# Kernel optimization log

Hardware: AMD Instinct MI355X
Metric: run time of the kernel (lower is better)

The kernel has to match this reference:

```python
import jax, jax.numpy as jnp
import numpy as np

L = 2        # n_layers
F = 128      # in_features == out_features (GRUCell + highway constraint)
O = 128
N = 1024     # nodes
B = 8        # batch
D = 3        # edge directions (weight.size(0))


def setup_inputs() -> dict:
    key = jax.random.key(0)
    ks = jax.random.split(key, 10)
    s = 1.0 / np.sqrt(F)
    u = lambda k, shp: jax.random.uniform(k, shp, jnp.float32, minval=-s, maxval=s)
    return {
        "inputs": jax.random.normal(ks[0], (N, B, F), jnp.float32),
        "adj": jax.random.uniform(ks[1], (D, B, N, N), jnp.float32),
        "W": u(ks[2], (L, D, F, O)),            # GCN weight per layer/direction
        "Bc": u(ks[3], (L, D, O)),              # GCN bias
        "Wh": u(ks[4], (L, F, O)),              # highway weight
        "Bh": u(ks[5], (L, O)),                 # highway bias
        "Wih": u(ks[6], (L, 3 * O, O)),         # GRUCell input weights
        "Whh": u(ks[7], (L, 3 * O, O)),         # GRUCell hidden weights
        "bih": u(ks[8], (L, 3 * O)),
        "bhh": u(ks[9], (L, 3 * O)),
    }


def _gru(x, h, wih, whh, bih, bhh):
    # torch.nn.GRUCell semantics; x,h: [..., O]
    gi = x @ wih.T + bih
    gh = h @ whh.T + bhh
    i_r, i_z, i_n = jnp.split(gi, 3, axis=-1)
    h_r, h_z, h_n = jnp.split(gh, 3, axis=-1)
    r = jax.nn.sigmoid(i_r + h_r)
    z = jax.nn.sigmoid(i_z + h_z)
    n = jnp.tanh(i_n + r * h_n)
    return (1.0 - z) * n + z * h


def reference(inputs, adj, W, Bc, Wh, Bh, Wih, Whh, bih, bhh):
    x = inputs  # [N, B, F]; dropout layers are identity at eval
    for l in range(L):
        # support per direction: [D, B, N, O]
        support = jnp.einsum('nbf,dfo->dbno', x, W[l]) + Bc[l][:, None, None, :]
        # adjacency-weighted aggregation: adj[d,b] @ support[d,b]
        agg = jnp.einsum('dbmn,dbno->dbmo', adj, support)
        # GRU update with hidden = current features, per direction, summed over d
        h = jnp.broadcast_to(jnp.transpose(x, (1, 0, 2))[None], agg.shape)
        hnew = _gru(agg, h, Wih[l], Whh[l], bih[l], bhh[l])
        out = jnp.transpose(jnp.sum(hnew, axis=0), (1, 0, 2))  # [N, B, O]
        out = jax.nn.relu(out)  # activation='relu'
        # highway gate (highway='relu')
        t = jax.nn.relu(jnp.einsum('nbf,fo->nbo', x, Wh[l]) + Bh[l])
        x = out * t + x * (1.0 - t)
    return x
```

## Files before the change

kernel.cpp:

```cpp
#include <hip/hip_runtime.h>
#include <math.h>

#define N_NODES 1024
#define BATCH   8
#define FEAT    128
#define NDIR    3
#define NB      (N_NODES*BATCH)
#define G3      384

typedef __bf16 bf16_t;
using bf16x8 = __attribute__((ext_vector_type(8))) __bf16;
using bf16x4 = __attribute__((ext_vector_type(4))) __bf16;
using f32x4  = __attribute__((ext_vector_type(4))) float;

#define GLOAD_LDS16(g, l) \
    __builtin_amdgcn_global_load_lds((const __attribute__((address_space(1))) void*)(g), \
                                     (__attribute__((address_space(3))) void*)(l), 16, 0, 0)

template<int R>
__device__ __forceinline__ void stage_swz(const bf16_t* __restrict__ src, int stride,
                                          int k0, bf16_t* lds, int w, int lane)
{
    #pragma unroll
    for (int q = 0; q < R/32; ++q) {
        int rbase = w*(R/4) + q*8;
        int row = rbase + (lane >> 3);
        int seg = (lane & 7) ^ (row & 7);
        GLOAD_LDS16(src + (size_t)row*stride + k0 + seg*8,
                    (char*)lds + (size_t)rbase*128);
    }
}

__device__ __forceinline__ void stageA_f32(const float* __restrict__ src, int k0,
                                           bf16_t* lds, bf16_t* __restrict__ gout,
                                           int w, int lane)
{
    #pragma unroll
    for (int q = 0; q < 2; ++q) {
        int rbase = w*16 + q*8;
        int row = rbase + (lane >> 3);
        int s   = lane & 7;
        int seg = s ^ (row & 7);
        const float* g = src + (size_t)row*1024 + k0 + seg*8;
        float4 v0 = *reinterpret_cast<const float4*>(g);
        float4 v1 = *reinterpret_cast<const float4*>(g + 4);
        bf16x8 pk;
        pk[0]=(bf16_t)(v0.x-0.5f); pk[1]=(bf16_t)(v0.y-0.5f);
        pk[2]=(bf16_t)(v0.z-0.5f); pk[3]=(bf16_t)(v0.w-0.5f);
        pk[4]=(bf16_t)(v1.x-0.5f); pk[5]=(bf16_t)(v1.y-0.5f);
        pk[6]=(bf16_t)(v1.z-0.5f); pk[7]=(bf16_t)(v1.w-0.5f);
        *reinterpret_cast<bf16x8*>(&lds[row*64 + s*8]) = pk;
        *reinterpret_cast<bf16x8*>(gout + (size_t)row*1024 + k0 + seg*8) = pk;
    }
}

template<int MI, int NJ>
__device__ __forceinline__ void mfma_swz(const bf16_t* As, const bf16_t* Bs,
                                         f32x4 (&acc)[MI][NJ], int wr, int wc, int lane)
{
    #pragma unroll
    for (int ks = 0; ks < 64; ks += 32) {
        int bslot = ks/8 + (lane >> 4);
        int sx = bslot ^ (lane & 7);
        bf16x8 af[MI], bfv[NJ];
        #pragma unroll
        for (int i = 0; i < MI; ++i) {
            int row = wr*MI*16 + i*16 + (lane & 15);
            af[i] = *reinterpret_cast<const bf16x8*>(&As[row*64 + sx*8]);
        }
        #pragma unroll
        for (int j = 0; j < NJ; ++j) {
            int row = wc*NJ*16 + j*16 + (lane & 15);
            bfv[j] = *reinterpret_cast<const bf16x8*>(&Bs[row*64 + sx*8]);
        }
        #pragma unroll
        for (int i = 0; i < MI; ++i) {
            #pragma unroll
            for (int j = 0; j < NJ; ++j)
                acc[i][j] = __builtin_amdgcn_mfma_f32_16x16x32_bf16(af[i], bfv[j], acc[i][j], 0, 0, 0);
        }
    }
}

__global__ __launch_bounds__(128) void k_wprep(
    const float* __restrict__ W, const float* __restrict__ Wh,
    const float* __restrict__ Whh, const float* __restrict__ Wih,
    bf16_t* __restrict__ wsup,
    bf16_t* __restrict__ wihc)
{
    int m = blockIdx.x, l = blockIdx.y, k = threadIdx.x;
    float w;
    bf16_t* dst;
    bool patB = false;
    if (m < 384) {
        int d = m >> 7, o = m & 127;
        w = W[((size_t)(l*3 + d)*128 + k)*128 + o];
        dst = wsup + ((size_t)l*896 + m)*384;
    } else if (m < 512) {
        int o = m - 384;
        w = Wh[((size_t)l*128 + k)*128 + o];
        dst = wsup + ((size_t)l*896 + m)*384;
    } else if (m < 896) {
        int c = m - 512;
        w = Whh[((size_t)l*384 + c)*128 + k];
        dst = wsup + ((size_t)l*896 + m)*384;
    } else {
        int c = m - 896;
        w = Wih[((size_t)l*384 + c)*128 + k];
        dst = wihc + ((size_t)l*384 + c)*384;
        patB = true;
    }
    bf16_t hi = (bf16_t)w;
    bf16_t lo = (bf16_t)(w - (float)hi);
    if (patB) { dst[k] = hi; dst[128 + k] = hi; dst[256 + k] = lo; }
    else      { dst[k] = hi; dst[128 + k] = lo; dst[256 + k] = hi; }
}

__global__ __launch_bounds__(256) void k_xcat(
    const float* __restrict__ X, bf16_t* __restrict__ xcat)
{
    int idx = blockIdx.x * 256 + threadIdx.x;
    int k = idx & 127, r = idx >> 7;
    int n = r >> 3, b = r & 7;
    float v = X[idx];
    bf16_t hi = (bf16_t)v;
    bf16_t lo = (bf16_t)(v - (float)hi);
    bf16_t* dst = xcat + ((size_t)(b*1024 + n))*384 + k;
    dst[0] = hi; dst[128] = hi; dst[256] = lo;
}

__global__ __launch_bounds__(256, 2) void k_sup2(
    const bf16_t* __restrict__ Wcat,
    const bf16_t* __restrict__ xcat,
    const float* __restrict__ Bcl,
    const float* __restrict__ Bhl,
    const float* __restrict__ bhhl,
    bf16_t* __restrict__ supt,
    float* __restrict__ tbuf,
    bf16_t* __restrict__ ghb)
{
    __shared__ bf16_t As[2][128*64];
    __shared__ bf16_t Bs[2][128*64];
    const int t = threadIdx.x, lane = t & 63, w = t >> 6;
    const int wr = w >> 1, wc = w & 1;
    const int n0 = blockIdx.x * 128;
    const int m0 = blockIdx.y * 128;
    const int b  = blockIdx.z;
    const bf16_t* Arow = Wcat + (size_t)m0 * 384;
    const bf16_t* Brow = xcat + ((size_t)b * 1024 + n0) * 384;

    f32x4 acc[4][4] = {};
    stage_swz<128>(Arow, 384, 0, As[0], w, lane);
    stage_swz<128>(Brow, 384, 0, Bs[0], w, lane);
    __syncthreads();
    #pragma unroll
    for (int kt = 0; kt < 6; ++kt) {
        if (kt + 1 < 6) {
            stage_swz<128>(Arow, 384, (kt+1)*64, As[(kt+1)&1], w, lane);
            stage_swz<128>(Brow, 384, (kt+1)*64, Bs[(kt+1)&1], w, lane);
        }
        mfma_swz<4,4>(As[kt&1], Bs[kt&1], acc, wr, wc, lane);
        __syncthreads();
    }
    #pragma unroll
    for (int i = 0; i < 4; ++i) {
        int mb = m0 + wr*64 + i*16 + ((lane >> 4) * 4);
        #pragma unroll
        for (int j = 0; j < 4; ++j) {
            int n = n0 + wc*64 + j*16 + (lane & 15);
            if (mb < 384) {
                #pragma unroll
                for (int rg = 0; rg < 4; ++rg) {
                    int m = mb + rg;
                    int d = m >> 7, o = m & 127;
                    supt[((size_t)((d*8 + b)*128 + o))*1024 + n] =
                        (bf16_t)(acc[i][j][rg] + Bcl[d*128 + o]);
                }
            } else if (mb < 512) {
                #pragma unroll
                for (int rg = 0; rg < 4; ++rg) {
                    int o = mb + rg - 384;
                    tbuf[((size_t)(b*128 + o))*1024 + n] =
                        fmaxf(acc[i][j][rg] + Bhl[o], 0.0f);
                }
            } else {
                int c = mb - 512;
                bf16x4 pk;
                #pragma unroll
                for (int rg = 0; rg < 4; ++rg)
                    pk[rg] = (bf16_t)(acc[i][j][rg] + bhhl[c + rg]);
                *reinterpret_cast<bf16x4*>(&ghb[((size_t)(b*1024 + n))*384 + c]) = pk;
            }
        }
    }
}

__global__ __launch_bounds__(256) void k_colsum(
    const bf16_t* __restrict__ supt, float* __restrict__ colsum)
{
    int row = blockIdx.x * 4 + (threadIdx.x >> 6);
    int lane = threadIdx.x & 63;
    const bf16_t* p = supt + (size_t)row * 1024 + lane * 16;
    bf16x8 v0 = *reinterpret_cast<const bf16x8*>(p);
    bf16x8 v1 = *reinterpret_cast<const bf16x8*>(p + 8);
    float s = 0.0f;
    #pragma unroll
    for (int i = 0; i < 8; ++i) s += (float)v0[i] + (float)v1[i];
    #pragma unroll
    for (int off = 32; off > 0; off >>= 1) s += __shfl_down(s, off, 64);
    if (lane == 0) colsum[row] = s;
}

template<int AMODE>
__global__ __launch_bounds__(256, 2) void k_agg(
    const float* __restrict__ adjf,
    bf16_t* __restrict__ adjb,
    const bf16_t* __restrict__ supt,
    const float* __restrict__ colsum,
    bf16_t* __restrict__ aggcat)
{
    __shared__ bf16_t As[2][64*64];
    __shared__ bf16_t Bs[2][128*64];
    const int t = threadIdx.x, lane = t & 63, w = t >> 6;
    const int wr = w >> 1, wc = w & 1;
    const int m0 = blockIdx.x * 64;
    const int z  = blockIdx.y;
    const float*  Af = adjf + (size_t)z * 1024 * 1024 + (size_t)m0 * 1024;
    bf16_t*       Ab = adjb + (size_t)z * 1024 * 1024 + (size_t)m0 * 1024;
    const bf16_t* Brow = supt + (size_t)z * 128 * 1024;

    f32x4 acc[2][4] = {};
    if (AMODE) stageA_f32(Af, 0, As[0], Ab, w, lane);
    else       stage_swz<64>(Ab, 1024, 0, As[0], w, lane);
    stage_swz<128>(Brow, 1024, 0, Bs[0], w, lane);
    __syncthreads();
    #pragma unroll
    for (int kt = 0; kt < 16; ++kt) {
        if (kt + 1 < 16) {
            if (AMODE) stageA_f32(Af, (kt+1)*64, As[(kt+1)&1], Ab, w, lane);
            else       stage_swz<64>(Ab, 1024, (kt+1)*64, As[(kt+1)&1], w, lane);
            stage_swz<128>(Brow, 1024, (kt+1)*64, Bs[(kt+1)&1], w, lane);
        }
        mfma_swz<2,4>(As[kt&1], Bs[kt&1], acc, wr, wc, lane);
        __syncthreads();
    }
    #pragma unroll
    for (int i = 0; i < 2; ++i) {
        #pragma unroll
        for (int rg = 0; rg < 4; ++rg) {
            size_t m = (size_t)z*1024 + m0 + wr*32 + i*16 + ((lane >> 4) * 4) + rg;
            bf16_t* row = aggcat + m*384;
            #pragma unroll
            for (int j = 0; j < 4; ++j) {
                int o = wc*64 + j*16 + (lane & 15);
                float v = acc[i][j][rg] + 0.5f * colsum[z*128 + o];
                bf16_t hi = (bf16_t)v;
                bf16_t lo = (bf16_t)(v - (float)hi);
                row[o] = hi; row[128 + o] = lo; row[256 + o] = hi;
            }
        }
    }
}

__global__ __launch_bounds__(256, 2) void k_gi(
    const bf16_t* __restrict__ A,
    const bf16_t* __restrict__ B,
    const float*  __restrict__ bias,
    bf16_t* __restrict__ girz,
    float* __restrict__ gin)
{
    __shared__ bf16_t As[2][128*64];
    __shared__ bf16_t Bs[2][128*64];
    const int t = threadIdx.x, lane = t & 63, w = t >> 6;
    const int wr = w >> 1, wc = w & 1;
    const int m0 = blockIdx.x * 128;
    const int c0 = blockIdx.y * 128;
    const bf16_t* Arow = A + (size_t)m0 * 384;
    const bf16_t* Brow = B + (size_t)c0 * 384;

    f32x4 acc[4][4] = {};
    stage_swz<128>(Arow, 384, 0, As[0], w, lane);
    stage_swz<128>(Brow, 384, 0, Bs[0], w, lane);
    __syncthreads();
    #pragma unroll
    for (int kt = 0; kt < 6; ++kt) {
        if (kt + 1 < 6) {
            stage_swz<128>(Arow, 384, (kt+1)*64, As[(kt+1)&1], w, lane);
            stage_swz<128>(Brow, 384, (kt+1)*64, Bs[(kt+1)&1], w, lane);
        }
        mfma_swz<4,4>(As[kt&1], Bs[kt&1], acc, wr, wc, lane);
        __syncthreads();
    }
    #pragma unroll
    for (int j = 0; j < 4; ++j) {
        int c = c0 + wc*64 + j*16 + (lane & 15);
        float bv = bias[c];
        #pragma unroll
        for (int i = 0; i < 4; ++i) {
            #pragma unroll
            for (int rg = 0; rg < 4; ++rg) {
                int m = m0 + wr*64 + i*16 + ((lane >> 4) * 4) + rg;
                float v = acc[i][j][rg] + bv;
                if (c < 256) girz[(size_t)m*256 + c] = (bf16_t)v;
                else         gin[(size_t)m*128 + (c - 256)] = v;
            }
        }
    }
}

__global__ __launch_bounds__(256) void k_gates(
    const bf16_t* __restrict__ girz, const float* __restrict__ gin,
    const bf16_t* __restrict__ ghb,
    bf16_t* xcat,
    const float* __restrict__ tbuf,
    float* __restrict__ Xout, int write_xcat)
{
    __shared__ float ts[128*17];
    const int b = blockIdx.y, n0 = blockIdx.x * 16;
    const int tid = threadIdx.x;
    {
        int o = tid >> 1, nh = (tid & 1) * 8;
        const float* src = tbuf + ((size_t)(b*128 + o))*1024 + n0 + nh;
        float4 v0 = *reinterpret_cast<const float4*>(src);
        float4 v1 = *reinterpret_cast<const float4*>(src + 4);
        float* dst = &ts[o*17 + nh];
        dst[0]=v0.x; dst[1]=v0.y; dst[2]=v0.z; dst[3]=v0.w;
        dst[4]=v1.x; dst[5]=v1.y; dst[6]=v1.z; dst[7]=v1.w;
    }
    __syncthreads();
    #pragma unroll
    for (int p = 0; p < 8; ++p) {
        int e = p*256 + tid;
        int nn = e >> 7, o = e & 127;
        int n = n0 + nn;
        size_t rb = (size_t)(b*1024 + n);
        bf16_t* xr = xcat + rb*384;
        float h = (float)xr[o] + (float)xr[256 + o];
        const bf16_t* ghr = ghb + rb*G3;
        float g_r = (float)ghr[o], g_z = (float)ghr[128+o], g_n = (float)ghr[256+o];
        float acc = 0.0f;
        #pragma unroll
        for (int d = 0; d < 3; ++d) {
            size_t rr = (size_t)((d*8 + b)*1024 + n);
            float i_r = (float)girz[rr*256 + o];
            float i_z = (float)girz[rr*256 + 128 + o];
            float i_n = gin[rr*128 + o];
            float rg = 1.0f / (1.0f + expf(-(i_r + g_r)));
            float zg = 1.0f / (1.0f + expf(-(i_z + g_z)));
            float ng = tanhf(i_n + rg * g_n);
            acc += (1.0f - zg) * ng + zg * h;
        }
        float outv = fmaxf(acc, 0.0f);
        float tg = ts[o*17 + nn];
        float res = outv * tg + h * (1.0f - tg);
        if (Xout) Xout[(size_t)(n*8 + b)*128 + o] = res;
        if (write_xcat) {
            bf16_t hi = (bf16_t)res;
            bf16_t lo = (bf16_t)(res - (float)hi);
            xr[o] = hi; xr[128 + o] = hi; xr[256 + o] = lo;
        }
    }
}

extern "C" void kernel_launch(void* const* d_in, const int* in_sizes, int n_in,
                              void* d_out, int out_size, void* d_ws, size_t ws_size,
                              hipStream_t stream) {
    const float* inputs = (const float*)d_in[0];
    const float* adj    = (const float*)d_in[1];
    const float* W      = (const float*)d_in[2];
    const float* Bc     = (const float*)d_in[3];
    const float* Wh     = (const float*)d_in[4];
    const float* Bh     = (const float*)d_in[5];
    const float* Wih    = (const float*)d_in[6];
    const float* Whh    = (const float*)d_in[7];
    const float* bih    = (const float*)d_in[8];
    const float* bhh    = (const float*)d_in[9];

    char* ws = (char*)d_ws;
    float*  tbuf   = (float*)ws;   ws += (size_t)8*128*1024*4;
    bf16_t* xcat   = (bf16_t*)ws;  ws += (size_t)8*1024*384*2;
    bf16_t* ghb    = (bf16_t*)ws;  ws += (size_t)NB*G3*2;
    bf16_t* supt   = (bf16_t*)ws;  ws += (size_t)24*128*1024*2;
    bf16_t* aggcat = (bf16_t*)ws;  ws += (size_t)3*NB*384*2;
    bf16_t* girz   = (bf16_t*)ws;  ws += (size_t)3*NB*256*2;
    float*  gin    = (float*)ws;   ws += (size_t)3*NB*128*4;
    float*  colsum = (float*)ws;   ws += (size_t)24*128*4;
    bf16_t* wsup   = (bf16_t*)ws;  ws += (size_t)2*896*384*2;
    bf16_t* wihc   = (bf16_t*)ws;  ws += (size_t)2*384*384*2;
    bf16_t* adjb   = (bf16_t*)ws;

    k_wprep<<<dim3(1280, 2), dim3(128), 0, stream>>>(W, Wh, Whh, Wih, wsup, wihc);
    k_xcat<<<dim3(4096), dim3(256), 0, stream>>>(inputs, xcat);

    for (int l = 0; l < 2; ++l) {
        k_sup2<<<dim3(8, 7, 8), dim3(256), 0, stream>>>(
            wsup + (size_t)l*896*384, xcat, Bc + l*3*128, Bh + l*128, bhh + l*G3,
            supt, tbuf, ghb);
        k_colsum<<<dim3(768), dim3(256), 0, stream>>>(supt, colsum);
        if (l == 0)
            k_agg<1><<<dim3(16, 24), dim3(256), 0, stream>>>(adj, adjb, supt, colsum, aggcat);
        else
            k_agg<0><<<dim3(16, 24), dim3(256), 0, stream>>>(adj, adjb, supt, colsum, aggcat);
        k_gi<<<dim3(192, 3), dim3(256), 0, stream>>>(
            aggcat, wihc + (size_t)l*384*384, bih + l*G3, girz, gin);
        k_gates<<<dim3(64, 8), dim3(256), 0, stream>>>(
            girz, gin, ghb, xcat, tbuf,
            (l == 1) ? (float*)d_out : (float*)nullptr, (l == 0) ? 1 : 0);
    }
}
```

Measured before the change: 331.9 us.

## Fuse colsum into support GEMM, drop bf16 adj cache, use fast gate math

The column-sum kernel is removed and its reduction is folded into the support GEMM epilogue through wave shuffles and atomicAdd into a buffer zeroed by the xcat kernel. The aggregation kernel now always converts fp32 adjacency on the fly instead of writing a bf16 copy in layer 0 and reading it back in layer 1. Its occupancy hint is raised to 3 blocks per SM, and the GRU gates use exp2/rcp intrinsics in place of expf/tanhf. This saves a kernel launch and the adjb write, but layer 1 now reads fp32 adjacency (twice the bytes), and the atomics make the sums order-dependent.

```diff
diff --git a/kernel.cpp b/kernel.cpp
--- a/kernel.cpp
+++ b/kernel.cpp
@@ -32,8 +32,7 @@
 }
 
 __device__ __forceinline__ void stageA_f32(const float* __restrict__ src, int k0,
-                                           bf16_t* lds, bf16_t* __restrict__ gout,
-                                           int w, int lane)
+                                           bf16_t* lds, int w, int lane)
 {
     #pragma unroll
     for (int q = 0; q < 2; ++q) {
@@ -50,7 +49,6 @@
         pk[4]=(bf16_t)(v1.x-0.5f); pk[5]=(bf16_t)(v1.y-0.5f);
         pk[6]=(bf16_t)(v1.z-0.5f); pk[7]=(bf16_t)(v1.w-0.5f);
         *reinterpret_cast<bf16x8*>(&lds[row*64 + s*8]) = pk;
-        *reinterpret_cast<bf16x8*>(gout + (size_t)row*1024 + k0 + seg*8) = pk;
     }
 }
 
@@ -80,6 +78,19 @@
                 acc[i][j] = __builtin_amdgcn_mfma_f32_16x16x32_bf16(af[i], bfv[j], acc[i][j], 0, 0, 0);
         }
     }
+}
+
+__device__ __forceinline__ float fast_sigmoid(float x)
+{
+    float t = __builtin_amdgcn_exp2f(-1.442695041f * x);
+    return __builtin_amdgcn_rcpf(1.0f + t);
+}
+__device__ __forceinline__ float fast_tanh(float x)
+{
+    float ax = fabsf(x);
+    float t = __builtin_amdgcn_exp2f(-2.885390082f * ax);
+    float r = (1.0f - t) * __builtin_amdgcn_rcpf(1.0f + t);
+    return copysignf(r, x);
 }
 
 __global__ __launch_bounds__(128) void k_wprep(
@@ -117,9 +128,11 @@
 }
 
 __global__ __launch_bounds__(256) void k_xcat(
-    const float* __restrict__ X, bf16_t* __restrict__ xcat)
+    const float* __restrict__ X, bf16_t* __restrict__ xcat,
+    float* __restrict__ colsum2)
 {
     int idx = blockIdx.x * 256 + threadIdx.x;
+    if (idx < 2*3072) colsum2[idx] = 0.0f;
     int k = idx & 127, r = idx >> 7;
     int n = r >> 3, b = r & 7;
     float v = X[idx];
@@ -137,7 +150,8 @@
     const float* __restrict__ bhhl,
     bf16_t* __restrict__ supt,
     float* __restrict__ tbuf,
-    bf16_t* __restrict__ ghb)
+    bf16_t* __restrict__ ghb,
+    float* __restrict__ colsum)
 {
     __shared__ bf16_t As[2][128*64];
     __shared__ bf16_t Bs[2][128*64];
@@ -165,25 +179,42 @@
     #pragma unroll
     for (int i = 0; i < 4; ++i) {
         int mb = m0 + wr*64 + i*16 + ((lane >> 4) * 4);
-        #pragma unroll
-        for (int j = 0; j < 4; ++j) {
-            int n = n0 + wc*64 + j*16 + (lane & 15);
-            if (mb < 384) {
+        if (mb < 384) {
+            #pragma unroll
+            for (int rg = 0; rg < 4; ++rg) {
+                int m = mb + rg;
+                int d = m >> 7, o = m & 127;
+                float bv = Bcl[d*128 + o];
+                float psum = 0.0f;
                 #pragma unroll
-                for (int rg = 0; rg < 4; ++rg) {
-                    int m = mb + rg;
-                    int d = m >> 7, o = m & 127;
-                    supt[((size_t)((d*8 + b)*128 + o))*1024 + n] =
-                        (bf16_t)(acc[i][j][rg] + Bcl[d*128 + o]);
+                for (int j = 0; j < 4; ++j) {
+                    int n = n0 + wc*64 + j*16 + (lane & 15);
+                    bf16_t sv = (bf16_t)(acc[i][j][rg] + bv);
+                    supt[((size_t)((d*8 + b)*128 + o))*1024 + n] = sv;
+                    psum += (float)sv;
                 }
-            } else if (mb < 512) {
+                psum += __shfl_xor(psum, 1, 64);
+                psum += __shfl_xor(psum, 2, 64);
+                psum += __shfl_xor(psum, 4, 64);
+                psum += __shfl_xor(psum, 8, 64);
+                if ((lane & 15) == 0)
+                    atomicAdd(&colsum[(d*8 + b)*128 + o], psum);
+            }
+        } else if (mb < 512) {
+            #pragma unroll
+            for (int j = 0; j < 4; ++j) {
+                int n = n0 + wc*64 + j*16 + (lane & 15);
                 #pragma unroll
                 for (int rg = 0; rg < 4; ++rg) {
                     int o = mb + rg - 384;
                     tbuf[((size_t)(b*128 + o))*1024 + n] =
                         fmaxf(acc[i][j][rg] + Bhl[o], 0.0f);
                 }
-            } else {
+            }
+        } else {
+            #pragma unroll
+            for (int j = 0; j < 4; ++j) {
+                int n = n0 + wc*64 + j*16 + (lane & 15);
                 int c = mb - 512;
                 bf16x4 pk;
                 #pragma unroll
@@ -195,26 +226,8 @@
     }
 }
 
-__global__ __launch_bounds__(256) void k_colsum(
-    const bf16_t* __restrict__ supt, float* __restrict__ colsum)
-{
-    int row = blockIdx.x * 4 + (threadIdx.x >> 6);
-    int lane = threadIdx.x & 63;
-    const bf16_t* p = supt + (size_t)row * 1024 + lane * 16;
-    bf16x8 v0 = *reinterpret_cast<const bf16x8*>(p);
-    bf16x8 v1 = *reinterpret_cast<const bf16x8*>(p + 8);
-    float s = 0.0f;
-    #pragma unroll
-    for (int i = 0; i < 8; ++i) s += (float)v0[i] + (float)v1[i];
-    #pragma unroll
-    for (int off = 32; off > 0; off >>= 1) s += __shfl_down(s, off, 64);
-    if (lane == 0) colsum[row] = s;
-}
-
-template<int AMODE>
-__global__ __launch_bounds__(256, 2) void k_agg(
+__global__ __launch_bounds__(256, 3) void k_agg(
     const float* __restrict__ adjf,
-    bf16_t* __restrict__ adjb,
     const bf16_t* __restrict__ supt,
     const float* __restrict__ colsum,
     bf16_t* __restrict__ aggcat)
@@ -226,19 +239,16 @@
     const int m0 = blockIdx.x * 64;
     const int z  = blockIdx.y;
     const float*  Af = adjf + (size_t)z * 1024 * 1024 + (size_t)m0 * 1024;
-    bf16_t*       Ab = adjb + (size_t)z * 1024 * 1024 + (size_t)m0 * 1024;
     const bf16_t* Brow = supt + (size_t)z * 128 * 1024;
 
     f32x4 acc[2][4] = {};
-    if (AMODE) stageA_f32(Af, 0, As[0], Ab, w, lane);
-    else       stage_swz<64>(Ab, 1024, 0, As[0], w, lane);
+    stageA_f32(Af, 0, As[0], w, lane);
     stage_swz<128>(Brow, 1024, 0, Bs[0], w, lane);
     __syncthreads();
     #pragma unroll
     for (int kt = 0; kt < 16; ++kt) {
         if (kt + 1 < 16) {
-            if (AMODE) stageA_f32(Af, (kt+1)*64, As[(kt+1)&1], Ab, w, lane);
-            else       stage_swz<64>(Ab, 1024, (kt+1)*64, As[(kt+1)&1], w, lane);
+            stageA_f32(Af, (kt+1)*64, As[(kt+1)&1], w, lane);
             stage_swz<128>(Brow, 1024, (kt+1)*64, Bs[(kt+1)&1], w, lane);
         }
         mfma_swz<2,4>(As[kt&1], Bs[kt&1], acc, wr, wc, lane);
@@ -345,9 +355,9 @@
             float i_r = (float)girz[rr*256 + o];
             float i_z = (float)girz[rr*256 + 128 + o];
             float i_n = gin[rr*128 + o];
-            float rg = 1.0f / (1.0f + expf(-(i_r + g_r)));
-            float zg = 1.0f / (1.0f + expf(-(i_z + g_z)));
-            float ng = tanhf(i_n + rg * g_n);
+            float rg = fast_sigmoid(i_r + g_r);
+            float zg = fast_sigmoid(i_z + g_z);
+            float ng = fast_tanh(i_n + rg * g_n);
             acc += (1.0f - zg) * ng + zg * h;
         }
         float outv = fmaxf(acc, 0.0f);
@@ -384,23 +394,19 @@
     bf16_t* aggcat = (bf16_t*)ws;  ws += (size_t)3*NB*384*2;
     bf16_t* girz   = (bf16_t*)ws;  ws += (size_t)3*NB*256*2;
     float*  gin    = (float*)ws;   ws += (size_t)3*NB*128*4;
-    float*  colsum = (float*)ws;   ws += (size_t)24*128*4;
+    float*  colsum2= (float*)ws;   ws += (size_t)2*24*128*4;
     bf16_t* wsup   = (bf16_t*)ws;  ws += (size_t)2*896*384*2;
-    bf16_t* wihc   = (bf16_t*)ws;  ws += (size_t)2*384*384*2;
-    bf16_t* adjb   = (bf16_t*)ws;
+    bf16_t* wihc   = (bf16_t*)ws;
 
     k_wprep<<<dim3(1280, 2), dim3(128), 0, stream>>>(W, Wh, Whh, Wih, wsup, wihc);
-    k_xcat<<<dim3(4096), dim3(256), 0, stream>>>(inputs, xcat);
+    k_xcat<<<dim3(4096), dim3(256), 0, stream>>>(inputs, xcat, colsum2);
 
     for (int l = 0; l < 2; ++l) {
+        float* colsum = colsum2 + l*3072;
         k_sup2<<<dim3(8, 7, 8), dim3(256), 0, stream>>>(
             wsup + (size_t)l*896*384, xcat, Bc + l*3*128, Bh + l*128, bhh + l*G3,
-            supt, tbuf, ghb);
-        k_colsum<<<dim3(768), dim3(256), 0, stream>>>(supt, colsum);
-        if (l == 0)
-            k_agg<1><<<dim3(16, 24), dim3(256), 0, stream>>>(adj, adjb, supt, colsum, aggcat);
-        else
-            k_agg<0><<<dim3(16, 24), dim3(256), 0, stream>>>(adj, adjb, supt, colsum, aggcat);
+            supt, tbuf, ghb, colsum);
+        k_agg<<<dim3(16, 24), dim3(256), 0, stream>>>(adj, supt, colsum, aggcat);
         k_gi<<<dim3(192, 3), dim3(256), 0, stream>>>(
             aggcat, wihc + (size_t)l*384*384, bih + l*G3, girz, gin);
         k_gates<<<dim3(64, 8), dim3(256), 0, stream>>>(
```

Measured after the change: 316.2 us. -4.7%, faster.
